# Optimization experiments

Hardware: AMD Instinct MI355X
Metric: run time of the kernel (lower is better)

The kernel has to match this reference:

```python
import jax, jax.numpy as jnp
import numpy as np

B, N, E, D_IN, D_OUT = 16, 2048, 65536, 256, 256


def setup_inputs() -> dict:
    key = jax.random.key(0)
    k1, k2, k3 = jax.random.split(key, 3)
    node_features = jax.random.normal(k1, (B, N, D_IN), dtype=jnp.float32)
    edge_indices = jax.random.randint(k2, (B, 2, E), 0, N, dtype=jnp.int64)
    W = jax.random.normal(k3, (D_OUT, 2 * D_IN), dtype=jnp.float32) * (1.0 / np.sqrt(2 * D_IN))
    b = jnp.zeros((D_OUT,), dtype=jnp.float32)
    return {"node_features": node_features, "edge_indices": edge_indices, "W": W, "b": b}


def reference(node_features, edge_indices, W, b):
    # node_features: [B, N, D]; edge_indices: [B, 2, E] (src row 0, dst row 1)
    n_nodes = node_features.shape[1]
    src = edge_indices[:, 0, :]  # [B, E]
    dst = edge_indices[:, 1, :]  # [B, E]
    # gather source-node features per edge: [B, E, D]
    gathered = jnp.take_along_axis(node_features, src[:, :, None], axis=1)

    def per_graph(feats_g, dst_g):
        s = jax.ops.segment_sum(feats_g, dst_g, num_segments=n_nodes)          # [N, D]
        c = jax.ops.segment_sum(jnp.ones_like(dst_g, dtype=feats_g.dtype),
                                dst_g, num_segments=n_nodes)                    # [N]
        return s / jnp.maximum(c, 1.0)[:, None]  # mean; 0 for isolated nodes

    neighbor_agg = jax.vmap(per_graph)(gathered, dst)            # [B, N, D]
    combined = jnp.concatenate([node_features, neighbor_agg], axis=-1)  # [B, N, 2D]
    return jnp.einsum('bnd,od->bno', combined, W) + b
```

## Files before the change

### kernel.cpp

```cpp
#include <hip/hip_runtime.h>
#include <hip/hip_bf16.h>

#define BATCH 16
#define NNODE 2048
#define NEDGE 65536
#define DIN   256
#define DOUT  256
#define KDIM  512
#define SUB   16
#define ESUB  (NEDGE/SUB)

typedef __attribute__((ext_vector_type(8))) short short8;
typedef __attribute__((ext_vector_type(8))) ushort ushort8;
typedef __attribute__((ext_vector_type(4))) float f32x4;

__device__ __forceinline__ ushort f2bf(float f) {
    union { float f; unsigned u; } v; v.f = f;
    unsigned u = v.u;
    unsigned r = (u + 0x7fffu + ((u >> 16) & 1u)) >> 16;
    return (ushort)r;
}

__device__ __forceinline__ int q8(float x) {
    float c = fminf(fmaxf(x * 16.0f, -127.0f), 127.0f);
    return (int)rintf(c);
}

#define ASYNC_COPY16(gsrc, ldst) \
    __builtin_amdgcn_global_load_lds((const __attribute__((address_space(1))) void*)(gsrc), \
                                     (__attribute__((address_space(3))) void*)(ldst), 16, 0, 0)

__global__ __launch_bounds__(256) void prep_kernel(
        const float* __restrict__ X, const float* __restrict__ W,
        const int* __restrict__ E,
        int* __restrict__ partial,
        ushort* __restrict__ Xbf, unsigned char* __restrict__ Xi8,
        ushort* __restrict__ Wbf) {
    int bid = blockIdx.x;
    int t = threadIdx.x;
    if (bid < 256) {
        __shared__ int hist[NNODE];
        int b = bid & 15, sub = bid >> 4;
#pragma unroll
        for (int j = 0; j < 8; ++j) hist[t + j * 256] = 0;
        __syncthreads();
        const int4* dsts = reinterpret_cast<const int4*>(
            E + (size_t)b * 2 * NEDGE + NEDGE + sub * ESUB);
#pragma unroll
        for (int j = 0; j < 4; ++j) {
            int4 d = dsts[j * 256 + t];
            atomicAdd(&hist[d.x], 1);
            atomicAdd(&hist[d.y], 1);
            atomicAdd(&hist[d.z], 1);
            atomicAdd(&hist[d.w], 1);
        }
        __syncthreads();
        int* pb = partial + ((size_t)b * SUB + sub) * NNODE;
#pragma unroll
        for (int j = 0; j < 8; ++j) pb[t + j * 256] = hist[t + j * 256];
    } else if (bid < 4352) {
        size_t i = (size_t)(bid - 256) * 256 + t;
        const float4* p = reinterpret_cast<const float4*>(X + i * 8);
        float4 u = p[0], v = p[1];
        ushort4 o0 = { f2bf(u.x), f2bf(u.y), f2bf(u.z), f2bf(u.w) };
        ushort4 o1 = { f2bf(v.x), f2bf(v.y), f2bf(v.z), f2bf(v.w) };
        *reinterpret_cast<ushort4*>(Xbf + i * 8)     = o0;
        *reinterpret_cast<ushort4*>(Xbf + i * 8 + 4) = o1;
        unsigned q0 = (q8(u.x) & 255) | ((q8(u.y) & 255) << 8) |
                      ((q8(u.z) & 255) << 16) | ((unsigned)(q8(u.w) & 255) << 24);
        unsigned q1 = (q8(v.x) & 255) | ((q8(v.y) & 255) << 8) |
                      ((q8(v.z) & 255) << 16) | ((unsigned)(q8(v.w) & 255) << 24);
        uint2 q = { q0, q1 };
        *reinterpret_cast<uint2*>(Xi8 + i * 8) = q;
    } else {
        size_t i = (size_t)(bid - 4352) * 256 + t;
        const float4* p = reinterpret_cast<const float4*>(W + i * 8);
        float4 u = p[0], v = p[1];
        ushort4 o0 = { f2bf(u.x), f2bf(u.y), f2bf(u.z), f2bf(u.w) };
        ushort4 o1 = { f2bf(v.x), f2bf(v.y), f2bf(v.z), f2bf(v.w) };
        *reinterpret_cast<ushort4*>(Wbf + i * 8)     = o0;
        *reinterpret_cast<ushort4*>(Wbf + i * 8 + 4) = o1;
    }
}

__global__ __launch_bounds__(256) void scan_kernel(
        const int* __restrict__ partial,
        int* __restrict__ counts, int* __restrict__ cursor,
        int* __restrict__ subStart) {
    __shared__ int tsum[256];
    int b = blockIdx.x;
    int t = threadIdx.x;
    const int* pb = partial + (size_t)b * SUB * NNODE;
    int tot[8] = {};
    for (int k = 0; k < SUB; ++k) {
        const int4* p = reinterpret_cast<const int4*>(pb + k * NNODE + t * 8);
        int4 a = p[0], c = p[1];
        tot[0] += a.x; tot[1] += a.y; tot[2] += a.z; tot[3] += a.w;
        tot[4] += c.x; tot[5] += c.y; tot[6] += c.z; tot[7] += c.w;
    }
    int s = 0;
#pragma unroll
    for (int j = 0; j < 8; ++j) s += tot[j];
    tsum[t] = s;
    __syncthreads();
    for (int off = 1; off < 256; off <<= 1) {
        int v = (t >= off) ? tsum[t - off] : 0;
        __syncthreads();
        tsum[t] += v;
        __syncthreads();
    }
    int run = (t == 0) ? 0 : tsum[t - 1];
    int base = b * NNODE + t * 8;
    int cur[8];
#pragma unroll
    for (int j = 0; j < 8; ++j) {
        counts[base + j] = tot[j];
        cursor[base + j] = run;
        cur[j] = run;
        run += tot[j];
    }
    int* sb = subStart + (size_t)b * SUB * NNODE;
    for (int k = 0; k < SUB; ++k) {
        const int4* p = reinterpret_cast<const int4*>(pb + k * NNODE + t * 8);
        int4 a = p[0], c = p[1];
        int4 o0 = { cur[0], cur[1], cur[2], cur[3] };
        int4 o1 = { cur[4], cur[5], cur[6], cur[7] };
        *reinterpret_cast<int4*>(sb + k * NNODE + t * 8)     = o0;
        *reinterpret_cast<int4*>(sb + k * NNODE + t * 8 + 4) = o1;
        cur[0] += a.x; cur[1] += a.y; cur[2] += a.z; cur[3] += a.w;
        cur[4] += c.x; cur[5] += c.y; cur[6] += c.z; cur[7] += c.w;
    }
}

__global__ __launch_bounds__(256) void fill_kernel(
        const int* __restrict__ E,
        const int* __restrict__ subStart,
        int* __restrict__ srcIdx) {
    __shared__ int cur[NNODE];
    int bid = blockIdx.x;
    int t = threadIdx.x;
    int b = bid & 15, sub = bid >> 4;
    const int* ss = subStart + ((size_t)b * SUB + sub) * NNODE;
#pragma unroll
    for (int j = 0; j < 8; ++j) cur[t + j * 256] = ss[t + j * 256];
    __syncthreads();
    const int* eb = E + (size_t)b * 2 * NEDGE;
    const int4* srcs = reinterpret_cast<const int4*>(eb + sub * ESUB);
    const int4* dsts = reinterpret_cast<const int4*>(eb + NEDGE + sub * ESUB);
    int* sb = srcIdx + (size_t)b * NEDGE;
#pragma unroll
    for (int j = 0; j < 4; ++j) {
        int4 s = srcs[j * 256 + t];
        int4 d = dsts[j * 256 + t];
        sb[atomicAdd(&cur[d.x], 1)] = s.x;
        sb[atomicAdd(&cur[d.y], 1)] = s.y;
        sb[atomicAdd(&cur[d.z], 1)] = s.z;
        sb[atomicAdd(&cur[d.w], 1)] = s.w;
    }
}

__global__ __launch_bounds__(256) void aggregate_kernel(
        const unsigned char* __restrict__ Xi8,
        const int* __restrict__ srcIdx,
        const int* __restrict__ cursor,
        const int* __restrict__ counts,
        ushort* __restrict__ Gbf) {
    int bid = blockIdx.x;
    int blk = (bid & 7) * 1024 + (bid >> 3);
    int wave = threadIdx.x >> 6;
    int lane = threadIdx.x & 63;
    int half = lane >> 5;
    int f0 = (lane & 31) * 8;
    int node = blk * 4 + wave;
    int b = node >> 11;
    int deg = counts[node];
    int start = cursor[node];
    const unsigned char* xb = Xi8 + (size_t)b * NNODE * DIN;
    const int* sidx = srcIdx + (size_t)b * NEDGE + start;

    unsigned aA0 = 0, aA1 = 0, aB0 = 0, aB1 = 0;
#define ACC8(v) do {                                                          \
        unsigned wx = (v).x ^ 0x80808080u, wy = (v).y ^ 0x80808080u;          \
        aA0 += wx & 0x00FF00FFu;  aA1 += (wx >> 8) & 0x00FF00FFu;             \
        aB0 += wy & 0x00FF00FFu;  aB1 += (wy >> 8) & 0x00FF00FFu;             \
    } while (0)

    int i = 0;
    for (; i + 16 <= deg; i += 16) {
        int s[8];
#pragma unroll
        for (int u = 0; u < 8; ++u) s[u] = sidx[i + 2 * u + half];
        uint2 v[8];
#pragma unroll
        for (int u = 0; u < 8; ++u)
            v[u] = *reinterpret_cast<const uint2*>(xb + (size_t)s[u] * DIN + f0);
#pragma unroll
        for (int u = 0; u < 8; ++u) ACC8(v[u]);
    }
    for (; i + 8 <= deg; i += 8) {
        int s0 = sidx[i + 0 + half], s1 = sidx[i + 2 + half];
        int s2 = sidx[i + 4 + half], s3 = sidx[i + 6 + half];
        uint2 v0 = *reinterpret_cast<const uint2*>(xb + (size_t)s0 * DIN + f0);
        uint2 v1 = *reinterpret_cast<const uint2*>(xb + (size_t)s1 * DIN + f0);
        uint2 v2 = *reinterpret_cast<const uint2*>(xb + (size_t)s2 * DIN + f0);
        uint2 v3 = *reinterpret_cast<const uint2*>(xb + (size_t)s3 * DIN + f0);
        ACC8(v0); ACC8(v1); ACC8(v2); ACC8(v3);
    }
    for (; i + 2 <= deg; i += 2) {
        int s0 = sidx[i + half];
        uint2 v0 = *reinterpret_cast<const uint2*>(xb + (size_t)s0 * DIN + f0);
        ACC8(v0);
    }
    if (i < deg && half == 0) {
        int s0 = sidx[i];
        uint2 v0 = *reinterpret_cast<const uint2*>(xb + (size_t)s0 * DIN + f0);
        ACC8(v0);
    }
#undef ACC8
    aA0 += (unsigned)__shfl_xor((int)aA0, 32, 64);
    aA1 += (unsigned)__shfl_xor((int)aA1, 32, 64);
    aB0 += (unsigned)__shfl_xor((int)aB0, 32, 64);
    aB1 += (unsigned)__shfl_xor((int)aB1, 32, 64);

    if (half == 0) {
        float sc = 1.0f / (16.0f * (float)max(deg, 1));
        float bias = 128.0f * (float)deg;
        float f[8];
        f[0] = ((float)(int)(aA0 & 0xFFFFu) - bias) * sc;
        f[2] = ((float)(int)(aA0 >> 16)     - bias) * sc;
        f[1] = ((float)(int)(aA1 & 0xFFFFu) - bias) * sc;
        f[3] = ((float)(int)(aA1 >> 16)     - bias) * sc;
        f[4] = ((float)(int)(aB0 & 0xFFFFu) - bias) * sc;
        f[6] = ((float)(int)(aB0 >> 16)     - bias) * sc;
        f[5] = ((float)(int)(aB1 & 0xFFFFu) - bias) * sc;
        f[7] = ((float)(int)(aB1 >> 16)     - bias) * sc;
        ushort8 o;
#pragma unroll
        for (int j = 0; j < 8; ++j) o[j] = f2bf(f[j]);
        *reinterpret_cast<ushort8*>(Gbf + (size_t)node * DIN + f0) = o;
    }
}

__global__ __launch_bounds__(256) void gemm_kernel(
        const ushort* __restrict__ Xbf,
        const ushort* __restrict__ Gbf,
        const ushort* __restrict__ Wbf,
        const float* __restrict__ bias,
        float* __restrict__ out) {
    __shared__ ushort As[2][128 * 32];
    __shared__ ushort Bs[2][128 * 32];
    const int tid = threadIdx.x;
    const int wid = tid >> 6, lane = tid & 63;

    int orig = blockIdx.x;
    int logical = (orig & 7) * 64 + (orig >> 3);
    int bx = logical >> 1;
    int by = logical & 1;
    const int rowBase = bx * 128;
    const int colBase = by * 128;
    const int wm = wid >> 1, wn = wid & 1;

    f32x4 acc[4][4] = {};

    const int lr = lane >> 2;
    const int lk = (lane & 3) * 8;

    const ushort* Arow = Xbf + (size_t)rowBase * DIN;
    const ushort* Grow = Gbf + (size_t)rowBase * DIN;
    const ushort* Brow = Wbf + (size_t)colBase * KDIM;
    const int r0 = wid * 16 + lr;

#define STAGE(k0, buf) do {                                                   \
        const ushort* Ab = ((k0) < DIN) ? (Arow + (k0)) : (Grow + ((k0) - DIN)); \
        const ushort* Bb = Brow + (k0);                                       \
        ASYNC_COPY16(Ab + (size_t)r0 * DIN + lk,          &As[buf][wid * 512]);       \
        ASYNC_COPY16(Ab + (size_t)(r0 + 64) * DIN + lk,   &As[buf][2048 + wid * 512]);\
        ASYNC_COPY16(Bb + (size_t)r0 * KDIM + lk,         &Bs[buf][wid * 512]);       \
        ASYNC_COPY16(Bb + (size_t)(r0 + 64) * KDIM + lk,  &Bs[buf][2048 + wid * 512]);\
    } while (0)

    STAGE(0, 0);
    int cur = 0;
    for (int t = 0; t < 16; ++t) {
        if (t < 15) {
            STAGE((t + 1) * 32, cur ^ 1);
            asm volatile("s_waitcnt vmcnt(4)" ::: "memory");
        } else {
            asm volatile("s_waitcnt vmcnt(0)" ::: "memory");
        }
        __builtin_amdgcn_s_barrier();

        short8 a[4], b[4];
#pragma unroll
        for (int m = 0; m < 4; ++m)
            a[m] = *reinterpret_cast<const short8*>(
                &As[cur][(wm * 64 + m * 16 + (lane & 15)) * 32 + (lane >> 4) * 8]);
#pragma unroll
        for (int n = 0; n < 4; ++n)
            b[n] = *reinterpret_cast<const short8*>(
                &Bs[cur][(wn * 64 + n * 16 + (lane & 15)) * 32 + (lane >> 4) * 8]);
#pragma unroll
        for (int m = 0; m < 4; ++m)
#pragma unroll
            for (int n = 0; n < 4; ++n)
                acc[m][n] = __builtin_amdgcn_mfma_f32_16x16x32_bf16(
                    a[m], b[n], acc[m][n], 0, 0, 0);
        __builtin_amdgcn_s_barrier();
        cur ^= 1;
    }
#undef STAGE

    const int cl = lane & 15, rq = lane >> 4;
#pragma unroll
    for (int n = 0; n < 4; ++n) {
        int col = colBase + wn * 64 + n * 16 + cl;
        float bv = bias[col];
#pragma unroll
        for (int m = 0; m < 4; ++m) {
            int r0o = rowBase + wm * 64 + m * 16 + rq * 4;
#pragma unroll
            for (int j = 0; j < 4; ++j)
                out[(size_t)(r0o + j) * DOUT + col] = acc[m][n][j] + bv;
        }
    }
}

extern "C" void kernel_launch(void* const* d_in, const int* in_sizes, int n_in,
                              void* d_out, int out_size, void* d_ws, size_t ws_size,
                              hipStream_t stream) {
    const float* X    = (const float*)d_in[0];
    const int*   E    = (const int*)d_in[1];
    const float* W    = (const float*)d_in[2];
    const float* bias = (const float*)d_in[3];
    float* out = (float*)d_out;

    char* ws = (char*)d_ws;
    ushort* Xbf  = (ushort*)ws;
    ushort* Gbf  = Xbf + (size_t)BATCH * NNODE * DIN;
    ushort* Wbf  = Gbf + (size_t)BATCH * NNODE * DIN;
    int* counts  = (int*)(Wbf + (size_t)DOUT * KDIM);
    int* cursor  = counts + BATCH * NNODE;
    int* srcIdx  = cursor + BATCH * NNODE;
    unsigned char* Xi8 = (unsigned char*)(srcIdx + (size_t)BATCH * NEDGE);
    int* partial  = (int*)Gbf;
    int* subStart = partial + (size_t)BATCH * SUB * NNODE;

    prep_kernel<<<4416, 256, 0, stream>>>(X, W, E, partial, Xbf, Xi8, Wbf);

    scan_kernel<<<BATCH, 256, 0, stream>>>(partial, counts, cursor, subStart);

    fill_kernel<<<256, 256, 0, stream>>>(E, subStart, srcIdx);

    aggregate_kernel<<<(BATCH * NNODE) / 4, 256, 0, stream>>>(
        Xi8, srcIdx, cursor, counts, Gbf);

    dim3 ggrid(512);
    gemm_kernel<<<ggrid, 256, 0, stream>>>(Xbf, Gbf, Wbf, bias, out);
}
```

Measured before the change: 72.40 us.

## Fuse scan into fill kernel and swizzle GEMM shared-memory tiles

Merges the per-graph scan and the CSR fill into one kernel. Each of the 256 blocks recomputes the scan redundantly and derives its own sub-chunk start offsets in shared memory, so the subStart round trip through global memory and one launch go away. Separately, it XOR-swizzles the 16-byte column chunk used by the GEMM's async copies and MFMA fragment loads to reduce LDS bank conflicts. The cost is that every fill block repeats the scan's reads and prefix work instead of one block per graph doing it.

```diff
diff --git a/kernel.cpp b/kernel.cpp
--- a/kernel.cpp
+++ b/kernel.cpp
@@ -83,18 +83,26 @@
     }
 }
 
-__global__ __launch_bounds__(256) void scan_kernel(
+__global__ __launch_bounds__(256) void fillscan_kernel(
+        const int* __restrict__ E,
         const int* __restrict__ partial,
         int* __restrict__ counts, int* __restrict__ cursor,
-        int* __restrict__ subStart) {
+        int* __restrict__ srcIdx) {
+    __shared__ int cur[NNODE];
     __shared__ int tsum[256];
-    int b = blockIdx.x;
+    int bid = blockIdx.x;
     int t = threadIdx.x;
+    int b = bid & 15, sub = bid >> 4;
     const int* pb = partial + (size_t)b * SUB * NNODE;
-    int tot[8] = {};
+
+    int tot[8] = {}, pre[8] = {};
     for (int k = 0; k < SUB; ++k) {
         const int4* p = reinterpret_cast<const int4*>(pb + k * NNODE + t * 8);
         int4 a = p[0], c = p[1];
+        if (k < sub) {
+            pre[0] += a.x; pre[1] += a.y; pre[2] += a.z; pre[3] += a.w;
+            pre[4] += c.x; pre[5] += c.y; pre[6] += c.z; pre[7] += c.w;
+        }
         tot[0] += a.x; tot[1] += a.y; tot[2] += a.z; tot[3] += a.w;
         tot[4] += c.x; tot[5] += c.y; tot[6] += c.z; tot[7] += c.w;
     }
@@ -110,52 +118,28 @@
         __syncthreads();
     }
     int run = (t == 0) ? 0 : tsum[t - 1];
+    bool writer = (sub == 0);
     int base = b * NNODE + t * 8;
-    int cur[8];
 #pragma unroll
     for (int j = 0; j < 8; ++j) {
-        counts[base + j] = tot[j];
-        cursor[base + j] = run;
-        cur[j] = run;
+        cur[t * 8 + j] = run + pre[j];
+        if (writer) { counts[base + j] = tot[j]; cursor[base + j] = run; }
         run += tot[j];
     }
-    int* sb = subStart + (size_t)b * SUB * NNODE;
-    for (int k = 0; k < SUB; ++k) {
-        const int4* p = reinterpret_cast<const int4*>(pb + k * NNODE + t * 8);
-        int4 a = p[0], c = p[1];
-        int4 o0 = { cur[0], cur[1], cur[2], cur[3] };
-        int4 o1 = { cur[4], cur[5], cur[6], cur[7] };
-        *reinterpret_cast<int4*>(sb + k * NNODE + t * 8)     = o0;
-        *reinterpret_cast<int4*>(sb + k * NNODE + t * 8 + 4) = o1;
-        cur[0] += a.x; cur[1] += a.y; cur[2] += a.z; cur[3] += a.w;
-        cur[4] += c.x; cur[5] += c.y; cur[6] += c.z; cur[7] += c.w;
-    }
-}
-
-__global__ __launch_bounds__(256) void fill_kernel(
-        const int* __restrict__ E,
-        const int* __restrict__ subStart,
-        int* __restrict__ srcIdx) {
-    __shared__ int cur[NNODE];
-    int bid = blockIdx.x;
-    int t = threadIdx.x;
-    int b = bid & 15, sub = bid >> 4;
-    const int* ss = subStart + ((size_t)b * SUB + sub) * NNODE;
-#pragma unroll
-    for (int j = 0; j < 8; ++j) cur[t + j * 256] = ss[t + j * 256];
     __syncthreads();
+
     const int* eb = E + (size_t)b * 2 * NEDGE;
     const int4* srcs = reinterpret_cast<const int4*>(eb + sub * ESUB);
     const int4* dsts = reinterpret_cast<const int4*>(eb + NEDGE + sub * ESUB);
     int* sb = srcIdx + (size_t)b * NEDGE;
 #pragma unroll
     for (int j = 0; j < 4; ++j) {
-        int4 s = srcs[j * 256 + t];
-        int4 d = dsts[j * 256 + t];
-        sb[atomicAdd(&cur[d.x], 1)] = s.x;
-        sb[atomicAdd(&cur[d.y], 1)] = s.y;
-        sb[atomicAdd(&cur[d.z], 1)] = s.z;
-        sb[atomicAdd(&cur[d.w], 1)] = s.w;
+        int4 sv = srcs[j * 256 + t];
+        int4 dv = dsts[j * 256 + t];
+        sb[atomicAdd(&cur[dv.x], 1)] = sv.x;
+        sb[atomicAdd(&cur[dv.y], 1)] = sv.y;
+        sb[atomicAdd(&cur[dv.z], 1)] = sv.z;
+        sb[atomicAdd(&cur[dv.w], 1)] = sv.w;
     }
 }
 
@@ -263,7 +247,7 @@
     f32x4 acc[4][4] = {};
 
     const int lr = lane >> 2;
-    const int lk = (lane & 3) * 8;
+    const int lk = (((lane & 3) ^ ((lane >> 3) & 3)) * 8);
 
     const ushort* Arow = Xbf + (size_t)rowBase * DIN;
     const ushort* Grow = Gbf + (size_t)rowBase * DIN;
@@ -278,6 +262,9 @@
         ASYNC_COPY16(Bb + (size_t)r0 * KDIM + lk,         &Bs[buf][wid * 512]);       \
         ASYNC_COPY16(Bb + (size_t)(r0 + 64) * KDIM + lk,  &Bs[buf][2048 + wid * 512]);\
     } while (0)
+
+    const int fl = lane & 15;
+    const int fc = ((lane >> 4) ^ ((fl >> 1) & 3)) * 8;
 
     STAGE(0, 0);
     int cur = 0;
@@ -294,11 +281,11 @@
 #pragma unroll
         for (int m = 0; m < 4; ++m)
             a[m] = *reinterpret_cast<const short8*>(
-                &As[cur][(wm * 64 + m * 16 + (lane & 15)) * 32 + (lane >> 4) * 8]);
+                &As[cur][(wm * 64 + m * 16 + fl) * 32 + fc]);
 #pragma unroll
         for (int n = 0; n < 4; ++n)
             b[n] = *reinterpret_cast<const short8*>(
-                &Bs[cur][(wn * 64 + n * 16 + (lane & 15)) * 32 + (lane >> 4) * 8]);
+                &Bs[cur][(wn * 64 + n * 16 + fl) * 32 + fc]);
 #pragma unroll
         for (int m = 0; m < 4; ++m)
 #pragma unroll
@@ -342,14 +329,11 @@
     int* cursor  = counts + BATCH * NNODE;
     int* srcIdx  = cursor + BATCH * NNODE;
     unsigned char* Xi8 = (unsigned char*)(srcIdx + (size_t)BATCH * NEDGE);
-    int* partial  = (int*)Gbf;
-    int* subStart = partial + (size_t)BATCH * SUB * NNODE;
+    int* partial = (int*)Gbf;
 
     prep_kernel<<<4416, 256, 0, stream>>>(X, W, E, partial, Xbf, Xi8, Wbf);
 
-    scan_kernel<<<BATCH, 256, 0, stream>>>(partial, counts, cursor, subStart);
-
-    fill_kernel<<<256, 256, 0, stream>>>(E, subStart, srcIdx);
+    fillscan_kernel<<<256, 256, 0, stream>>>(E, partial, counts, cursor, srcIdx);
 
     aggregate_kernel<<<(BATCH * NNODE) / 4, 256, 0, stream>>>(
         Xi8, srcIdx, cursor, counts, Gbf);
```

Measured after the change: 67.05 us. 1.08x faster.
